# Kernel tuning notes

Measured on AMD Instinct MI355X. Metric: run time of the kernel, lower is better.

The kernel has to match this reference:

```python
import jax, jax.numpy as jnp
import numpy as np

RANK = 16
ALPHA = 32.0
SCALING = ALPHA / RANK  # 2.0


def setup_inputs() -> dict:
    key = jax.random.key(0)
    k1, k2, k3, k4, k5 = jax.random.split(key, 5)
    B, S, D_IN, D_OUT = 4, 4096, 4096, 4096
    x = jax.random.normal(k1, (B, S, D_IN), dtype=jnp.float32)
    W = jax.random.normal(k2, (D_OUT, D_IN), dtype=jnp.float32) * 0.02
    b = jax.random.normal(k3, (D_OUT,), dtype=jnp.float32) * 0.02
    lora_A = jax.random.normal(k4, (RANK, D_IN), dtype=jnp.float32) * 0.02
    lora_B = jax.random.normal(k5, (D_OUT, RANK), dtype=jnp.float32) * 0.02
    return {"x": x, "W": W, "b": b, "lora_A": lora_A, "lora_B": lora_B}


def reference(x, W, b, lora_A, lora_B):
    # Base linear: y = x @ W^T + b
    base = jnp.einsum("bsd,od->bso", x, W) + b
    # LoRA delta: mathematically x @ (B @ A)^T * scaling == ((x @ A^T) @ B^T) * scaling.
    # We chain the two small rank-limited GEMMs (same math, efficient form).
    xa = jnp.einsum("bsd,rd->bsr", x, lora_A)           # [B,S,rank]
    lora_out = jnp.einsum("bsr,or->bso", xa, lora_B)    # [B,S,out]
    return base + SCALING * lora_out
```

## Files before the change

### kernel.cpp

```cpp
#include <hip/hip_runtime.h>
#include <hip/hip_bf16.h>
#include <cstdint>

constexpr int  KDIM  = 4096;
constexpr int  NDIM  = 4096;
constexpr long MDIM  = 16384;
constexpr int  RANK_ = 16;
constexpr float SCALE_ = 2.0f;

constexpr int BK = 64;
constexpr int NT = KDIM / BK;

using bf16x8 = __attribute__((ext_vector_type(8))) short;
using f32x4  = __attribute__((ext_vector_type(4))) float;

__device__ __forceinline__ void gload_lds16(const void* g, void* l) {
  __builtin_amdgcn_global_load_lds(
      (const __attribute__((address_space(1))) void*)g,
      (__attribute__((address_space(3))) void*)l, 16, 0, 0);
}

__device__ __forceinline__ unsigned short f2bf(float f) {
  union { float f; unsigned u; } v; v.f = f;
  unsigned r = v.u + 0x7FFFu + ((v.u >> 16) & 1u);
  return (unsigned short)(r >> 16);
}

__global__ __launch_bounds__(256) void prep_w_kernel(
    const float* __restrict__ W, const float* __restrict__ lA,
    const float* __restrict__ lB, unsigned short* __restrict__ Wp) {
  const long total8 = (long)NDIM * KDIM / 8;
  for (long t = blockIdx.x * (long)blockDim.x + threadIdx.x; t < total8;
       t += (long)gridDim.x * blockDim.x) {
    const int o  = (int)(t / (KDIM / 8));
    const int d8 = (int)(t % (KDIM / 8)) * 8;
    const float4* w4 = reinterpret_cast<const float4*>(W + (size_t)o * KDIM + d8);
    float4 w0 = w4[0], w1 = w4[1];
    float acc[8] = {w0.x, w0.y, w0.z, w0.w, w1.x, w1.y, w1.z, w1.w};
#pragma unroll
    for (int r = 0; r < RANK_; ++r) {
      const float br = SCALE_ * lB[o * RANK_ + r];
      const float4* a4 = reinterpret_cast<const float4*>(lA + (size_t)r * KDIM + d8);
      float4 a0 = a4[0], a1 = a4[1];
      acc[0] += br * a0.x; acc[1] += br * a0.y; acc[2] += br * a0.z; acc[3] += br * a0.w;
      acc[4] += br * a1.x; acc[5] += br * a1.y; acc[6] += br * a1.z; acc[7] += br * a1.w;
    }
    uint4 o4;
    o4.x = (unsigned)f2bf(acc[0]) | ((unsigned)f2bf(acc[1]) << 16);
    o4.y = (unsigned)f2bf(acc[2]) | ((unsigned)f2bf(acc[3]) << 16);
    o4.z = (unsigned)f2bf(acc[4]) | ((unsigned)f2bf(acc[5]) << 16);
    o4.w = (unsigned)f2bf(acc[6]) | ((unsigned)f2bf(acc[7]) << 16);
    *reinterpret_cast<uint4*>(Wp + t * 8) = o4;
  }
}

__global__ __launch_bounds__(256) void conv_x_kernel(
    const float* __restrict__ x, unsigned short* __restrict__ xb) {
  const long total8 = MDIM * KDIM / 8;
  for (long t = blockIdx.x * (long)blockDim.x + threadIdx.x; t < total8;
       t += (long)gridDim.x * blockDim.x) {
    const float4* p = reinterpret_cast<const float4*>(x + t * 8);
    float4 a = p[0], b = p[1];
    uint4 o4;
    o4.x = (unsigned)f2bf(a.x) | ((unsigned)f2bf(a.y) << 16);
    o4.y = (unsigned)f2bf(a.z) | ((unsigned)f2bf(a.w) << 16);
    o4.z = (unsigned)f2bf(b.x) | ((unsigned)f2bf(b.y) << 16);
    o4.w = (unsigned)f2bf(b.z) | ((unsigned)f2bf(b.w) << 16);
    *reinterpret_cast<uint4*>(xb + t * 8) = o4;
  }
}

__global__ __launch_bounds__(512, 2) void gemm256_kernel(
    const unsigned short* __restrict__ A,
    const unsigned short* __restrict__ Bm,
    const float* __restrict__ bias,
    float* __restrict__ C) {
  __shared__ __align__(16) unsigned char lds[131072];

  const int tid  = threadIdx.x;
  const int wave = tid >> 6, lane = tid & 63;
  const int wm = wave >> 2, wn = wave & 3;
  const int r16 = lane & 15, hi = lane >> 4;
  const int swz5 = ((r16 >> 3) & 1) << 5;

  const int orig = blockIdx.x;
  const int bid  = (orig & 7) * 128 + (orig >> 3);
  const int bcol = (bid & 15) * 256;
  const int brow = (bid >> 4) * 256;

  const int st_row = wave * 16 + (lane >> 2);
  const int st_col = ((lane & 3) * 8) ^ (((lane >> 5) & 1) << 4);
  const unsigned short* Asrc = A  + (size_t)(brow + st_row) * KDIM + st_col;
  const unsigned short* Bsrc = Bm + (size_t)(bcol + st_row) * KDIM + st_col;
  unsigned char* const dwave = lds + wave * 1024;

  auto stage = [&](int tau, int s) {
    const unsigned short* g = (s >= 2 ? Asrc + (size_t)(s - 2) * 128 * KDIM
                                      : Bsrc + (size_t)s * 128 * KDIM) + tau * BK;
    unsigned char* d = dwave + (tau & 1) * 65536 + s * 16384;
    gload_lds16(g,      d);
    gload_lds16(g + 32, d + 8192);
  };

  auto ldfrag = [&](const unsigned char* half, int lrow, int kk) -> bf16x8 {
    return *reinterpret_cast<const bf16x8*>(
        half + kk * 8192 + lrow * 64 + (hi * 16 ^ swz5));
  };

  f32x4 acc[8][4];
#pragma unroll
  for (int m = 0; m < 8; ++m)
#pragma unroll
    for (int n = 0; n < 4; ++n) acc[m][n] = (f32x4){0.f, 0.f, 0.f, 0.f};

#pragma unroll
  for (int h = 0; h < 6; ++h) stage(h >> 2, h & 3);
  asm volatile("s_waitcnt vmcnt(4)" ::: "memory");
  __builtin_amdgcn_s_barrier();

  bf16x8 a[4][2], bl[2][2], bh[2][2];

  for (int t = 0; t < NT; ++t) {
    const unsigned char* buf = lds + (t & 1) * 65536;
    const unsigned char* Ah = buf + (2 + wm) * 16384;
    const unsigned char* Bh = buf + (wn >> 1) * 16384;
    const int lrB = (wn & 1) * 64;

#pragma unroll
    for (int m = 0; m < 4; ++m) {
      a[m][0] = ldfrag(Ah, m * 16 + r16, 0);
      a[m][1] = ldfrag(Ah, m * 16 + r16, 1);
    }
#pragma unroll
    for (int n = 0; n < 2; ++n) {
      bl[n][0] = ldfrag(Bh, lrB + n * 16 + r16, 0);
      bl[n][1] = ldfrag(Bh, lrB + n * 16 + r16, 1);
    }
    if (t + 1 < NT) stage(t + 1, 2);
    __builtin_amdgcn_s_barrier();
    asm volatile("s_waitcnt lgkmcnt(0)" ::: "memory");
    __builtin_amdgcn_s_setprio(1);
#pragma unroll
    for (int m = 0; m < 4; ++m)
#pragma unroll
      for (int n = 0; n < 2; ++n)
#pragma unroll
        for (int kk = 0; kk < 2; ++kk)
          acc[m][n] = __builtin_amdgcn_mfma_f32_16x16x32_bf16(
              a[m][kk], bl[n][kk], acc[m][n], 0, 0, 0);
    __builtin_amdgcn_s_setprio(0);
    __builtin_amdgcn_s_barrier();

#pragma unroll
    for (int n = 0; n < 2; ++n) {
      bh[n][0] = ldfrag(Bh, lrB + (n + 2) * 16 + r16, 0);
      bh[n][1] = ldfrag(Bh, lrB + (n + 2) * 16 + r16, 1);
    }
    if (t + 1 < NT) stage(t + 1, 3);
    __builtin_amdgcn_s_barrier();
    asm volatile("s_waitcnt lgkmcnt(0)" ::: "memory");
    __builtin_amdgcn_s_setprio(1);
#pragma unroll
    for (int m = 0; m < 4; ++m)
#pragma unroll
      for (int n = 0; n < 2; ++n)
#pragma unroll
        for (int kk = 0; kk < 2; ++kk)
          acc[m][n + 2] = __builtin_amdgcn_mfma_f32_16x16x32_bf16(
              a[m][kk], bh[n][kk], acc[m][n + 2], 0, 0, 0);
    __builtin_amdgcn_s_setprio(0);
    __builtin_amdgcn_s_barrier();

#pragma unroll
    for (int m = 0; m < 4; ++m) {
      a[m][0] = ldfrag(Ah, (m + 4) * 16 + r16, 0);
      a[m][1] = ldfrag(Ah, (m + 4) * 16 + r16, 1);
    }
    if (t + 2 < NT) stage(t + 2, 0);
    __builtin_amdgcn_s_barrier();
    asm volatile("s_waitcnt lgkmcnt(0)" ::: "memory");
    __builtin_amdgcn_s_setprio(1);
#pragma unroll
    for (int m = 0; m < 4; ++m)
#pragma unroll
      for (int n = 0; n < 2; ++n)
#pragma unroll
        for (int kk = 0; kk < 2; ++kk)
          acc[m + 4][n + 2] = __builtin_amdgcn_mfma_f32_16x16x32_bf16(
              a[m][kk], bh[n][kk], acc[m + 4][n + 2], 0, 0, 0);
    __builtin_amdgcn_s_setprio(0);
    __builtin_amdgcn_s_barrier();

    if (t + 2 < NT) stage(t + 2, 1);
    __builtin_amdgcn_s_barrier();
    __builtin_amdgcn_s_setprio(1);
#pragma unroll
    for (int m = 0; m < 4; ++m)
#pragma unroll
      for (int n = 0; n < 2; ++n)
#pragma unroll
        for (int kk = 0; kk < 2; ++kk)
          acc[m + 4][n] = __builtin_amdgcn_mfma_f32_16x16x32_bf16(
              a[m][kk], bl[n][kk], acc[m + 4][n], 0, 0, 0);
    __builtin_amdgcn_s_setprio(0);
    if (t < NT - 2)       asm volatile("s_waitcnt vmcnt(4)" ::: "memory");
    else if (t == NT - 2) asm volatile("s_waitcnt vmcnt(0)" ::: "memory");
    __builtin_amdgcn_s_barrier();
  }

#pragma unroll
  for (int n = 0; n < 4; ++n) {
    const int col = bcol + wn * 64 + n * 16 + r16;
    const float bv = bias[col];
#pragma unroll
    for (int m = 0; m < 8; ++m) {
      const size_t row0 = (size_t)brow + wm * 128 + m * 16 + hi * 4;
#pragma unroll
      for (int j = 0; j < 4; ++j)
        C[(row0 + j) * NDIM + col] = acc[m][n][j] + bv;
    }
  }
}

extern "C" void kernel_launch(void* const* d_in, const int* in_sizes, int n_in,
                              void* d_out, int out_size, void* d_ws, size_t ws_size,
                              hipStream_t stream) {
  const float* x  = (const float*)d_in[0];
  const float* W  = (const float*)d_in[1];
  const float* b  = (const float*)d_in[2];
  const float* lA = (const float*)d_in[3];
  const float* lB = (const float*)d_in[4];
  float* out = (float*)d_out;

  unsigned short* xb = (unsigned short*)d_ws;
  unsigned short* Wp = (unsigned short*)((char*)d_ws + (size_t)MDIM * KDIM * 2);

  conv_x_kernel<<<2048, 256, 0, stream>>>(x, xb);
  prep_w_kernel<<<2048, 256, 0, stream>>>(W, lA, lB, Wp);

  gemm256_kernel<<<1024, 512, 0, stream>>>(xb, Wp, b, out);
}
```

Baseline: 642.0 us.

## Restructure GEMM main loop pipeline and swap MFMA operands for vectorized stores

Replaces the staggered per-quarter global-to-LDS staging, which ran two tiles ahead, with a single stage of the whole next tile issued mid-iteration. The main loop is reorganised so that X fragments for the next tile are prefetched across the loop boundary, and each MFMA phase splits its k halves so it can start before all fragments have arrived. The MFMA operands are swapped so each lane holds four consecutive output columns. The epilogue then writes C and reads bias as 16-byte vectors instead of scalar strided stores. The trade-off is less prefetch depth, since only one tile is in flight, plus a full vmcnt(0) wait every iteration.

After: 744.8 us. +16.0%, slower.

```diff
diff --git a/kernel.cpp b/kernel.cpp
--- a/kernel.cpp
+++ b/kernel.cpp
@@ -92,14 +92,19 @@
   const int st_col = ((lane & 3) * 8) ^ (((lane >> 5) & 1) << 4);
   const unsigned short* Asrc = A  + (size_t)(brow + st_row) * KDIM + st_col;
   const unsigned short* Bsrc = Bm + (size_t)(bcol + st_row) * KDIM + st_col;
-  unsigned char* const dwave = lds + wave * 1024;
-
-  auto stage = [&](int tau, int s) {
-    const unsigned short* g = (s >= 2 ? Asrc + (size_t)(s - 2) * 128 * KDIM
-                                      : Bsrc + (size_t)s * 128 * KDIM) + tau * BK;
-    unsigned char* d = dwave + (tau & 1) * 65536 + s * 16384;
-    gload_lds16(g,      d);
-    gload_lds16(g + 32, d + 8192);
+
+  auto stageAll = [&](int tau) {
+    unsigned char* d0 = lds + ((tau & 1) << 16) + (wave << 10);
+    const unsigned short* ga = Asrc + (size_t)tau * BK;
+    const unsigned short* gb = Bsrc + (size_t)tau * BK;
+    gload_lds16(gb,                          d0);
+    gload_lds16(gb + 32,                     d0 + 8192);
+    gload_lds16(gb + (size_t)128 * KDIM,     d0 + 16384);
+    gload_lds16(gb + (size_t)128 * KDIM + 32, d0 + 16384 + 8192);
+    gload_lds16(ga,                          d0 + 32768);
+    gload_lds16(ga + 32,                     d0 + 32768 + 8192);
+    gload_lds16(ga + (size_t)128 * KDIM,     d0 + 49152);
+    gload_lds16(ga + (size_t)128 * KDIM + 32, d0 + 49152 + 8192);
   };
 
   auto ldfrag = [&](const unsigned char* half, int lrow, int kk) -> bf16x8 {
@@ -113,111 +118,128 @@
 #pragma unroll
     for (int n = 0; n < 4; ++n) acc[m][n] = (f32x4){0.f, 0.f, 0.f, 0.f};
 
-#pragma unroll
-  for (int h = 0; h < 6; ++h) stage(h >> 2, h & 3);
-  asm volatile("s_waitcnt vmcnt(4)" ::: "memory");
+  stageAll(0);
+  asm volatile("s_waitcnt vmcnt(0)" ::: "memory");
   __builtin_amdgcn_s_barrier();
 
-  bf16x8 a[4][2], bl[2][2], bh[2][2];
+  bf16x8 xlo0[4], xlo1[4], xh[4][2], wlo[2][2], wlo2[2][2], wh[2][2];
+  {
+    const unsigned char* Ah0 = lds + (2 + wm) * 16384;
+#pragma unroll
+    for (int m = 0; m < 4; ++m) xlo0[m] = ldfrag(Ah0, m * 16 + r16, 0);
+  }
+
+  const int lrB = (wn & 1) * 64;
 
   for (int t = 0; t < NT; ++t) {
-    const unsigned char* buf = lds + (t & 1) * 65536;
-    const unsigned char* Ah = buf + (2 + wm) * 16384;
-    const unsigned char* Bh = buf + (wn >> 1) * 16384;
-    const int lrB = (wn & 1) * 64;
-
-#pragma unroll
-    for (int m = 0; m < 4; ++m) {
-      a[m][0] = ldfrag(Ah, m * 16 + r16, 0);
-      a[m][1] = ldfrag(Ah, m * 16 + r16, 1);
-    }
+    const unsigned char* buf  = lds + ((t & 1) << 16);
+    const unsigned char* bufn = lds + (((t + 1) & 1) << 16);
+    const unsigned char* Ah   = buf  + (2 + wm) * 16384;
+    const unsigned char* AhN  = bufn + (2 + wm) * 16384;
+    const unsigned char* Bh   = buf  + (wn >> 1) * 16384;
+
 #pragma unroll
     for (int n = 0; n < 2; ++n) {
-      bl[n][0] = ldfrag(Bh, lrB + n * 16 + r16, 0);
-      bl[n][1] = ldfrag(Bh, lrB + n * 16 + r16, 1);
-    }
-    if (t + 1 < NT) stage(t + 1, 2);
-    __builtin_amdgcn_s_barrier();
-    asm volatile("s_waitcnt lgkmcnt(0)" ::: "memory");
-    __builtin_amdgcn_s_setprio(1);
-#pragma unroll
-    for (int m = 0; m < 4; ++m)
-#pragma unroll
-      for (int n = 0; n < 2; ++n)
-#pragma unroll
-        for (int kk = 0; kk < 2; ++kk)
-          acc[m][n] = __builtin_amdgcn_mfma_f32_16x16x32_bf16(
-              a[m][kk], bl[n][kk], acc[m][n], 0, 0, 0);
-    __builtin_amdgcn_s_setprio(0);
-    __builtin_amdgcn_s_barrier();
+      wlo[n][0] = ldfrag(Bh, lrB + n * 16 + r16, 0);
+      wlo[n][1] = ldfrag(Bh, lrB + n * 16 + r16, 1);
+    }
+#pragma unroll
+    for (int m = 0; m < 4; ++m) xlo1[m] = ldfrag(Ah, m * 16 + r16, 1);
+    asm volatile("" ::: "memory");
+    __builtin_amdgcn_s_barrier();
+    __builtin_amdgcn_s_setprio(1);
+#pragma unroll
+    for (int m = 0; m < 4; ++m)
+#pragma unroll
+      for (int n = 0; n < 2; ++n)
+        acc[m][n] = __builtin_amdgcn_mfma_f32_16x16x32_bf16(
+            wlo[n][0], xlo0[m], acc[m][n], 0, 0, 0);
+#pragma unroll
+    for (int m = 0; m < 4; ++m)
+#pragma unroll
+      for (int n = 0; n < 2; ++n)
+        acc[m][n] = __builtin_amdgcn_mfma_f32_16x16x32_bf16(
+            wlo[n][1], xlo1[m], acc[m][n], 0, 0, 0);
+    __builtin_amdgcn_s_setprio(0);
 
 #pragma unroll
     for (int n = 0; n < 2; ++n) {
-      bh[n][0] = ldfrag(Bh, lrB + (n + 2) * 16 + r16, 0);
-      bh[n][1] = ldfrag(Bh, lrB + (n + 2) * 16 + r16, 1);
-    }
-    if (t + 1 < NT) stage(t + 1, 3);
-    __builtin_amdgcn_s_barrier();
-    asm volatile("s_waitcnt lgkmcnt(0)" ::: "memory");
-    __builtin_amdgcn_s_setprio(1);
-#pragma unroll
-    for (int m = 0; m < 4; ++m)
-#pragma unroll
-      for (int n = 0; n < 2; ++n)
-#pragma unroll
-        for (int kk = 0; kk < 2; ++kk)
-          acc[m][n + 2] = __builtin_amdgcn_mfma_f32_16x16x32_bf16(
-              a[m][kk], bh[n][kk], acc[m][n + 2], 0, 0, 0);
-    __builtin_amdgcn_s_setprio(0);
-    __builtin_amdgcn_s_barrier();
-
-#pragma unroll
-    for (int m = 0; m < 4; ++m) {
-      a[m][0] = ldfrag(Ah, (m + 4) * 16 + r16, 0);
-      a[m][1] = ldfrag(Ah, (m + 4) * 16 + r16, 1);
-    }
-    if (t + 2 < NT) stage(t + 2, 0);
-    __builtin_amdgcn_s_barrier();
-    asm volatile("s_waitcnt lgkmcnt(0)" ::: "memory");
-    __builtin_amdgcn_s_setprio(1);
-#pragma unroll
-    for (int m = 0; m < 4; ++m)
-#pragma unroll
-      for (int n = 0; n < 2; ++n)
-#pragma unroll
-        for (int kk = 0; kk < 2; ++kk)
-          acc[m + 4][n + 2] = __builtin_amdgcn_mfma_f32_16x16x32_bf16(
-              a[m][kk], bh[n][kk], acc[m + 4][n + 2], 0, 0, 0);
-    __builtin_amdgcn_s_setprio(0);
-    __builtin_amdgcn_s_barrier();
-
-    if (t + 2 < NT) stage(t + 2, 1);
-    __builtin_amdgcn_s_barrier();
-    __builtin_amdgcn_s_setprio(1);
-#pragma unroll
-    for (int m = 0; m < 4; ++m)
-#pragma unroll
-      for (int n = 0; n < 2; ++n)
-#pragma unroll
-        for (int kk = 0; kk < 2; ++kk)
-          acc[m + 4][n] = __builtin_amdgcn_mfma_f32_16x16x32_bf16(
-              a[m][kk], bl[n][kk], acc[m + 4][n], 0, 0, 0);
-    __builtin_amdgcn_s_setprio(0);
-    if (t < NT - 2)       asm volatile("s_waitcnt vmcnt(4)" ::: "memory");
-    else if (t == NT - 2) asm volatile("s_waitcnt vmcnt(0)" ::: "memory");
-    __builtin_amdgcn_s_barrier();
+      wh[n][0] = ldfrag(Bh, lrB + (n + 2) * 16 + r16, 0);
+      wh[n][1] = ldfrag(Bh, lrB + (n + 2) * 16 + r16, 1);
+    }
+#pragma unroll
+    for (int m = 0; m < 4; ++m) xh[m][0] = ldfrag(Ah, (m + 4) * 16 + r16, 0);
+    if (t + 1 < NT) stageAll(t + 1);
+    asm volatile("" ::: "memory");
+    __builtin_amdgcn_s_barrier();
+    __builtin_amdgcn_s_setprio(1);
+#pragma unroll
+    for (int m = 0; m < 4; ++m)
+#pragma unroll
+      for (int n = 0; n < 2; ++n)
+        acc[m][n + 2] = __builtin_amdgcn_mfma_f32_16x16x32_bf16(
+            wh[n][0], xlo0[m], acc[m][n + 2], 0, 0, 0);
+#pragma unroll
+    for (int m = 0; m < 4; ++m)
+#pragma unroll
+      for (int n = 0; n < 2; ++n)
+        acc[m][n + 2] = __builtin_amdgcn_mfma_f32_16x16x32_bf16(
+            wh[n][1], xlo1[m], acc[m][n + 2], 0, 0, 0);
+    __builtin_amdgcn_s_setprio(0);
+
+#pragma unroll
+    for (int m = 0; m < 4; ++m) xh[m][1] = ldfrag(Ah, (m + 4) * 16 + r16, 1);
+    asm volatile("" ::: "memory");
+    __builtin_amdgcn_s_barrier();
+    __builtin_amdgcn_s_setprio(1);
+#pragma unroll
+    for (int m = 0; m < 4; ++m)
+#pragma unroll
+      for (int n = 0; n < 2; ++n)
+        acc[m + 4][n + 2] = __builtin_amdgcn_mfma_f32_16x16x32_bf16(
+            wh[n][0], xh[m][0], acc[m + 4][n + 2], 0, 0, 0);
+#pragma unroll
+    for (int m = 0; m < 4; ++m)
+#pragma unroll
+      for (int n = 0; n < 2; ++n)
+        acc[m + 4][n + 2] = __builtin_amdgcn_mfma_f32_16x16x32_bf16(
+            wh[n][1], xh[m][1], acc[m + 4][n + 2], 0, 0, 0);
+    __builtin_amdgcn_s_setprio(0);
+
+#pragma unroll
+    for (int n = 0; n < 2; ++n) {
+      wlo2[n][0] = ldfrag(Bh, lrB + n * 16 + r16, 0);
+      wlo2[n][1] = ldfrag(Bh, lrB + n * 16 + r16, 1);
+    }
+    asm volatile("s_waitcnt vmcnt(0)" ::: "memory");
+    __builtin_amdgcn_s_barrier();
+#pragma unroll
+    for (int m = 0; m < 4; ++m) xlo0[m] = ldfrag(AhN, m * 16 + r16, 0);
+    __builtin_amdgcn_s_setprio(1);
+#pragma unroll
+    for (int m = 0; m < 4; ++m)
+#pragma unroll
+      for (int n = 0; n < 2; ++n)
+        acc[m + 4][n] = __builtin_amdgcn_mfma_f32_16x16x32_bf16(
+            wlo2[n][0], xh[m][0], acc[m + 4][n], 0, 0, 0);
+#pragma unroll
+    for (int m = 0; m < 4; ++m)
+#pragma unroll
+      for (int n = 0; n < 2; ++n)
+        acc[m + 4][n] = __builtin_amdgcn_mfma_f32_16x16x32_bf16(
+            wlo2[n][1], xh[m][1], acc[m + 4][n], 0, 0, 0);
+    __builtin_amdgcn_s_setprio(0);
   }
 
 #pragma unroll
   for (int n = 0; n < 4; ++n) {
-    const int col = bcol + wn * 64 + n * 16 + r16;
-    const float bv = bias[col];
+    const int colb = bcol + wn * 64 + n * 16 + hi * 4;
+    const f32x4 bv = *reinterpret_cast<const f32x4*>(&bias[colb]);
 #pragma unroll
     for (int m = 0; m < 8; ++m) {
-      const size_t row0 = (size_t)brow + wm * 128 + m * 16 + hi * 4;
-#pragma unroll
-      for (int j = 0; j < 4; ++j)
-        C[(row0 + j) * NDIM + col] = acc[m][n][j] + bv;
+      const size_t row = (size_t)brow + wm * 128 + m * 16 + r16;
+      f32x4 v = acc[m][n] + bv;
+      *reinterpret_cast<f32x4*>(&C[row * NDIM + colb]) = v;
     }
   }
 }
```
